# Kernel optimization log

Hardware: AMD Instinct MI355X
Metric: run time of the kernel (lower is better)

The kernel has to match this reference:

```python
import jax, jax.numpy as jnp
import numpy as np

B, D = 64, 1024  # batch, feature dim (DINOv2 ViT-L/14 -> 1024 channels)


def setup_inputs() -> dict:
    key = jax.random.key(0)
    k1, k2 = jax.random.split(key)
    x1 = jax.random.normal(k1, (B, D), dtype=jnp.float32)
    x2 = jax.random.normal(k2, (B, D), dtype=jnp.float32)
    return {"x1": x1, "x2": x2}


def reference(x1, x2):
    # dca_similarity: per-sample centered outer-product covariance,
    # normalized by the product of unbiased stds. Vectorized over batch.
    d = x1.shape[1]
    x1c = x1 - jnp.mean(x1, axis=1, keepdims=True)          # [B, D]
    x2c = x2 - jnp.mean(x2, axis=1, keepdims=True)          # [B, D]
    x1_std = jnp.std(x1, axis=1, ddof=1, keepdims=True)     # [B, 1] (unbiased)
    x2_std = jnp.std(x2, axis=1, ddof=1, keepdims=True)     # [B, 1]
    # cov[b, i, j] = x1c[b, i] * x2c[b, j] / (D - 1)
    cov = jnp.einsum('bi,bj->bij', x1c, x2c) / jnp.float32(d - 1)
    std_prod = (x1_std * x2_std)[:, :, None]                # [B, 1, 1]
    return cov / std_prod
```

## Files before the change

kernel.cpp:

```cpp
#include <hip/hip_runtime.h>
#include <math.h>

#define BATCH 64
#define DIM   1024
#define ROWS_PER_BLOCK 4

__global__ __launch_bounds__(256) void dca_stats_kernel(
    const float* __restrict__ x1, const float* __restrict__ x2,
    float* __restrict__ wa, float* __restrict__ wb) {
    const int b = blockIdx.x;
    const int t = threadIdx.x;

    const float4 v1 = reinterpret_cast<const float4*>(x1 + b * DIM)[t];
    const float4 v2 = reinterpret_cast<const float4*>(x2 + b * DIM)[t];

    float s1 = v1.x + v1.y + v1.z + v1.w;
    float q1 = v1.x * v1.x + v1.y * v1.y + v1.z * v1.z + v1.w * v1.w;
    float s2 = v2.x + v2.y + v2.z + v2.w;
    float q2 = v2.x * v2.x + v2.y * v2.y + v2.z * v2.z + v2.w * v2.w;

    #pragma unroll
    for (int off = 32; off > 0; off >>= 1) {
        s1 += __shfl_xor(s1, off);
        q1 += __shfl_xor(q1, off);
        s2 += __shfl_xor(s2, off);
        q2 += __shfl_xor(q2, off);
    }

    __shared__ float red[4][4];
    __shared__ float bc[3];
    const int wave = t >> 6;
    const int lane = t & 63;
    if (lane == 0) {
        red[wave][0] = s1; red[wave][1] = q1;
        red[wave][2] = s2; red[wave][3] = q2;
    }
    __syncthreads();
    if (t == 0) {
        float S1 = 0.f, Q1 = 0.f, S2 = 0.f, Q2 = 0.f;
        #pragma unroll
        for (int w = 0; w < 4; ++w) {
            S1 += red[w][0]; Q1 += red[w][1];
            S2 += red[w][2]; Q2 += red[w][3];
        }
        const float invD = 1.0f / (float)DIM;
        const float m1 = S1 * invD;
        const float m2 = S2 * invD;
        float var1 = (Q1 - (float)DIM * m1 * m1) / (float)(DIM - 1);
        float var2 = (Q2 - (float)DIM * m2 * m2) / (float)(DIM - 1);
        var1 = fmaxf(var1, 0.0f);
        var2 = fmaxf(var2, 0.0f);
        const float scale = 1.0f / ((float)(DIM - 1) * sqrtf(var1) * sqrtf(var2));
        bc[0] = m1; bc[1] = m2; bc[2] = scale;
    }
    __syncthreads();
    const float m1 = bc[0], m2 = bc[1], sc = bc[2];

    float4 a4, b4;
    a4.x = (v1.x - m1) * sc; a4.y = (v1.y - m1) * sc;
    a4.z = (v1.z - m1) * sc; a4.w = (v1.w - m1) * sc;
    b4.x = v2.x - m2; b4.y = v2.y - m2;
    b4.z = v2.z - m2; b4.w = v2.w - m2;
    reinterpret_cast<float4*>(wa + b * DIM)[t] = a4;
    reinterpret_cast<float4*>(wb + b * DIM)[t] = b4;
}

__global__ __launch_bounds__(256) void dca_outer_kernel(
    const float* __restrict__ wa, const float* __restrict__ wb,
    float* __restrict__ out) {
    const int blk = blockIdx.x;
    const int row0 = blk * ROWS_PER_BLOCK;
    const int b = row0 >> 10;

    const float4 v = reinterpret_cast<const float4*>(wb + (b << 10))[threadIdx.x];

    #pragma unroll
    for (int r = 0; r < ROWS_PER_BLOCK; ++r) {
        const float a = wa[row0 + r];
        float4 o;
        o.x = a * v.x; o.y = a * v.y; o.z = a * v.z; o.w = a * v.w;
        reinterpret_cast<float4*>(out + ((size_t)(row0 + r) << 10))[threadIdx.x] = o;
    }
}

extern "C" void kernel_launch(void* const* d_in, const int* in_sizes, int n_in,
                              void* d_out, int out_size, void* d_ws, size_t ws_size,
                              hipStream_t stream) {
    const float* x1 = (const float*)d_in[0];
    const float* x2 = (const float*)d_in[1];
    float* out = (float*)d_out;

    float* wa = (float*)d_ws;
    float* wb = wa + BATCH * DIM;

    dca_stats_kernel<<<BATCH, 256, 0, stream>>>(x1, x2, wa, wb);
    dca_outer_kernel<<<(BATCH * DIM) / ROWS_PER_BLOCK, 256, 0, stream>>>(wa, wb, out);
}
```

Measured before the change: 260.4 us.

## Fuse stats and outer-product kernels, recomputing row statistics per block

Merges the statistics kernel and the outer-product kernel into one launch. Every block now reloads its batch row of x1 and x2, recomputes mean and std, and writes eight output rows instead of four. This removes a kernel launch and the workspace round trip. In exchange the reduction is repeated redundantly in 8192 blocks, but the inputs are small and cache-resident while the 256MB output write dominates.

```diff
diff --git a/kernel.cpp b/kernel.cpp
--- a/kernel.cpp
+++ b/kernel.cpp
@@ -3,13 +3,16 @@
 
 #define BATCH 64
 #define DIM   1024
-#define ROWS_PER_BLOCK 4
+#define ROWS_PER_BLOCK 8
 
-__global__ __launch_bounds__(256) void dca_stats_kernel(
+__global__ __launch_bounds__(256) void dca_fused_kernel(
     const float* __restrict__ x1, const float* __restrict__ x2,
-    float* __restrict__ wa, float* __restrict__ wb) {
-    const int b = blockIdx.x;
-    const int t = threadIdx.x;
+    float* __restrict__ out) {
+    const int blk  = blockIdx.x;
+    const int row0 = blk * ROWS_PER_BLOCK;
+    const int b    = row0 >> 10;
+    const int i0   = row0 & (DIM - 1);
+    const int t    = threadIdx.x;
 
     const float4 v1 = reinterpret_cast<const float4*>(x1 + b * DIM)[t];
     const float4 v2 = reinterpret_cast<const float4*>(x2 + b * DIM)[t];
@@ -56,30 +59,20 @@
     __syncthreads();
     const float m1 = bc[0], m2 = bc[1], sc = bc[2];
 
-    float4 a4, b4;
-    a4.x = (v1.x - m1) * sc; a4.y = (v1.y - m1) * sc;
-    a4.z = (v1.z - m1) * sc; a4.w = (v1.w - m1) * sc;
-    b4.x = v2.x - m2; b4.y = v2.y - m2;
-    b4.z = v2.z - m2; b4.w = v2.w - m2;
-    reinterpret_cast<float4*>(wa + b * DIM)[t] = a4;
-    reinterpret_cast<float4*>(wb + b * DIM)[t] = b4;
-}
+    float4 w;
+    w.x = v2.x - m2; w.y = v2.y - m2; w.z = v2.z - m2; w.w = v2.w - m2;
 
-__global__ __launch_bounds__(256) void dca_outer_kernel(
-    const float* __restrict__ wa, const float* __restrict__ wb,
-    float* __restrict__ out) {
-    const int blk = blockIdx.x;
-    const int row0 = blk * ROWS_PER_BLOCK;
-    const int b = row0 >> 10;
-
-    const float4 v = reinterpret_cast<const float4*>(wb + (b << 10))[threadIdx.x];
+    const float* x1row = x1 + b * DIM + i0;
+    float a[ROWS_PER_BLOCK];
+    #pragma unroll
+    for (int r = 0; r < ROWS_PER_BLOCK; ++r)
+        a[r] = (x1row[r] - m1) * sc;
 
     #pragma unroll
     for (int r = 0; r < ROWS_PER_BLOCK; ++r) {
-        const float a = wa[row0 + r];
         float4 o;
-        o.x = a * v.x; o.y = a * v.y; o.z = a * v.z; o.w = a * v.w;
-        reinterpret_cast<float4*>(out + ((size_t)(row0 + r) << 10))[threadIdx.x] = o;
+        o.x = a[r] * w.x; o.y = a[r] * w.y; o.z = a[r] * w.z; o.w = a[r] * w.w;
+        reinterpret_cast<float4*>(out + ((size_t)(row0 + r) << 10))[t] = o;
     }
 }
 
@@ -90,9 +83,5 @@
     const float* x2 = (const float*)d_in[1];
     float* out = (float*)d_out;
 
-    float* wa = (float*)d_ws;
-    float* wb = wa + BATCH * DIM;
-
-    dca_stats_kernel<<<BATCH, 256, 0, stream>>>(x1, x2, wa, wb);
-    dca_outer_kernel<<<(BATCH * DIM) / ROWS_PER_BLOCK, 256, 0, stream>>>(wa, wb, out);
+    dca_fused_kernel<<<(BATCH * DIM) / ROWS_PER_BLOCK, 256, 0, stream>>>(x1, x2, out);
 }
```

New measurement: 258.1 us. About the same (-0.9%).
